# Kernel tuning notes

Hardware: AMD Instinct MI355X
Metric: run time of the kernel (lower is better)

## Reference

```python
import jax, jax.numpy as jnp
import numpy as np

K = 0.1            # manifold curvature param: points satisfy <x,x>_L = -1/K
H = 8              # num_heads
DH = 64            # head_spatial_dim
SP = 512           # spatial_dim = H*DH
SCALE = 1.0 / np.sqrt(DH)
SQRT_K = np.sqrt(K).astype(np.float32)


def _lorentz_fc(x, W, b):
    # Manifold-constrained FC: linear map to spatial coords, time recomputed
    sp = x @ W + b                                            # [..., out_spatial]
    t = jnp.sqrt(jnp.clip(1.0 / K + jnp.sum(sp * sp, axis=-1, keepdims=True), 1e-9, None))
    return jnp.concatenate([t, sp], axis=-1)


def _logmap0(p):
    # Lorentz log map at origin -> tangent spatial coords (time comp = 0)
    t, sp = p[..., :1], p[..., 1:]
    nrm = jnp.sqrt(jnp.sum(sp * sp, axis=-1, keepdims=True))
    theta = jnp.arccosh(jnp.clip(SQRT_K * t, 1.0 + 1e-7, None))
    return (theta / SQRT_K) * sp / jnp.maximum(nrm, 1e-9)


def _expmap0(u):
    nrm = jnp.sqrt(jnp.sum(u * u, axis=-1, keepdims=True))
    t = jnp.cosh(SQRT_K * nrm) / SQRT_K
    sp = jnp.sinh(SQRT_K * nrm) * u / (SQRT_K * jnp.maximum(nrm, 1e-9))
    return jnp.concatenate([t, sp], axis=-1)


def setup_inputs() -> dict:
    key = jax.random.key(0)
    ks = jax.random.split(key, 9)
    B, N = 4, 2048
    space = jax.random.normal(ks[0], (B, N, SP), dtype=jnp.float32) * 0.5
    t = jnp.sqrt(1.0 / K + jnp.sum(space * space, axis=-1, keepdims=True))
    x = jnp.concatenate([t, space], axis=-1)                  # on-manifold [B,N,513]
    s = (1 + SP) ** -0.5
    Wq = jax.random.normal(ks[1], (1 + SP, SP), dtype=jnp.float32) * s
    Wk = jax.random.normal(ks[2], (1 + SP, SP), dtype=jnp.float32) * s
    Wv = jax.random.normal(ks[3], (1 + SP, SP), dtype=jnp.float32) * s
    Wo = jax.random.normal(ks[4], (1 + SP, SP), dtype=jnp.float32) * s
    bq = jax.random.normal(ks[5], (SP,), dtype=jnp.float32) * 0.01
    bk = jax.random.normal(ks[6], (SP,), dtype=jnp.float32) * 0.01
    bv = jax.random.normal(ks[7], (SP,), dtype=jnp.float32) * 0.01
    bo = jax.random.normal(ks[8], (SP,), dtype=jnp.float32) * 0.01
    return {"x": x, "Wq": Wq, "bq": bq, "Wk": Wk, "bk": bk, "Wv": Wv, "bv": bv, "Wo": Wo, "bo": bo}


def _split_heads(p):
    # [B,N,1+H*DH] -> [B,H,N,1+DH], sharing the time component across heads
    B, N, _ = p.shape
    t = p[..., :1]                                            # [B,N,1]
    sp = p[..., 1:].reshape(B, N, H, DH)
    t = jnp.broadcast_to(t[:, :, None, :], (B, N, H, 1))
    return jnp.concatenate([t, sp], axis=-1).transpose(0, 2, 1, 3)


def reference(x, Wq, bq, Wk, bk, Wv, bv, Wo, bo):
    q = _split_heads(_lorentz_fc(x, Wq, bq))                  # [B,H,N,1+DH]
    k = _split_heads(_lorentz_fc(x, Wk, bk))
    v = _split_heads(_lorentz_fc(x, Wv, bv))
    # Lorentzian inner product scores: -q_t k_t + <q_s, k_s>
    scores = (jnp.einsum('bhnd,bhmd->bhnm', q[..., 1:], k[..., 1:])
              - jnp.einsum('bhni,bhmi->bhnm', q[..., :1], k[..., :1])) * SCALE
    attn = jax.nn.softmax(scores, axis=-1)                    # [B,H,N,N]
    # Riemannian aggregation: logmap0 -> weighted sum in tangent space -> expmap0
    v_tan = _logmap0(v)                                       # [B,H,N,DH]
    out_tan = jnp.einsum('bhnm,bhmd->bhnd', attn, v_tan)
    out = _expmap0(out_tan)                                   # [B,H,N,1+DH]
    # direct head concat: stack spatial parts, renormalize time onto manifold
    B, _, N, _ = out.shape
    space_cat = out[..., 1:].transpose(0, 2, 1, 3).reshape(B, N, H * DH)
    t_prime = jnp.sqrt(jnp.clip(1.0 / K + jnp.sum(space_cat * space_cat, axis=-1, keepdims=True), 1e-9, None))
    cat = jnp.concatenate([t_prime, space_cat], axis=-1)      # [B,N,513]
    return _lorentz_fc(cat, Wo, bo)                           # [B,N,513]
```

## Files before the change

### kernel.cpp

```cpp
#include <hip/hip_runtime.h>
#include <math.h>

#define H_    8
#define DH_   64
#define SPD   512
#define NSEQ  2048
#define BATCH 4
#define ROWS  8192
#define KDIM  513
#define INVK  10.0f
#define SQRTK 0.31622776601683794f
#define S2C   0.18033688011112043f
#define LOG2E 1.4426950408889634f
#define TKOFF 12.0f

using bf16x8 = __attribute__((ext_vector_type(8))) short;
using f32x4  = __attribute__((ext_vector_type(4))) float;
using f32x16 = __attribute__((ext_vector_type(16))) float;

static __device__ __forceinline__ short f2bf(float f){
  union { float f; unsigned u; } v; v.f = f;
  unsigned r = v.u + 0x7fffu + ((v.u >> 16) & 1u);
  return (short)(r >> 16);
}
static __device__ __forceinline__ float bf2f(short s){
  union { unsigned u; float f; } v; v.u = ((unsigned)(unsigned short)s) << 16;
  return v.f;
}
static __device__ __forceinline__ unsigned cvtpk(float lo, float hi){
  unsigned r; asm("v_cvt_pk_bf16_f32 %0, %1, %2" : "=v"(r) : "v"(lo), "v"(hi)); return r;
}
static __device__ __forceinline__ void plswapu(unsigned& a, unsigned& b){
  asm("v_permlane32_swap_b32 %0, %1" : "+v"(a), "+v"(b));
}
static __device__ __forceinline__ float exp2v(float x){
  float r; asm("v_exp_f32 %0, %1" : "=v"(r) : "v"(x)); return r;
}

#define GL16(gp, lp) __builtin_amdgcn_global_load_lds( \
    (const __attribute__((address_space(1))) void*)(gp), \
    (__attribute__((address_space(3))) void*)(lp), 16, 0, 0)

__global__ __launch_bounds__(256) void conv_kernel(const float* __restrict__ x,
                                                   const float* __restrict__ Wq,
                                                   const float* __restrict__ Wk,
                                                   const float* __restrict__ Wv,
                                                   const float* __restrict__ Wo,
                                                   short* __restrict__ xs,
                                                   short* __restrict__ WT){
  const int bid = blockIdx.x;
  if (bid < 8192){
    const int i2 = (bid * 256 + threadIdx.x) * 2;
    const int r = i2 >> 9, c = i2 & 511;
    const float a = x[(size_t)r * KDIM + 1 + c];
    const float b = x[(size_t)r * KDIM + 2 + c];
    const unsigned pk = (unsigned)(unsigned short)f2bf(a) |
                        ((unsigned)(unsigned short)f2bf(b) << 16);
    *(unsigned*)(xs + (size_t)r * SPD + c) = pk;
  } else {
    const int q = bid - 8192;
    const int wsel = q >> 10;
    const float* W = (wsel == 0) ? Wq : (wsel == 1) ? Wk : (wsel == 2) ? Wv : Wo;
    const int i = (q & 1023) * 256 + threadIdx.x;
    const int n = i >> 9, k = i & 511;
    WT[(size_t)wsel * SPD * SPD + i] = f2bf(W[(size_t)(k + 1) * SPD + n]);
  }
}

template<bool BF16OUT, int BM, bool TSQ, bool FUSESSQ>
__global__ __launch_bounds__(256) void gemm_kernel(
    const short* __restrict__ A, const short* __restrict__ WTbase,
    int sel0, int sel1, int sel2,
    const float* __restrict__ bias0, const float* __restrict__ bias1,
    const float* __restrict__ bias2,
    const float* __restrict__ W00, const float* __restrict__ W01,
    const float* __restrict__ W02,
    const float* __restrict__ tvec, long tstride,
    float* __restrict__ ssqout,
    void* __restrict__ C0, void* __restrict__ C1, void* __restrict__ C2,
    int ldc, int coff)
{
  constexpr int NREP = (BM == 128) ? 4 : 2;
  const int z = blockIdx.z;
  const int sel = (z == 0) ? sel0 : (z == 1) ? sel1 : sel2;
  const short* BT = WTbase + (size_t)sel * SPD * SPD;
  const float* bias = (z == 0) ? bias0 : (z == 1) ? bias1 : bias2;
  const float* W0 = (z == 0) ? W00 : (z == 1) ? W01 : W02;
  void* C = (z == 0) ? C0 : (z == 1) ? C1 : C2;

  __shared__ short As[BM * 32];
  __shared__ short Bs[128 * 32];

  const int tid  = threadIdx.x;
  const int lane = tid & 63;
  const int wave = tid >> 6;
  const int row0 = blockIdx.x * BM;
  const int col0 = blockIdx.y * 128;
  const int wr = (BM == 128) ? (wave >> 1) * 64 : 0;
  const int wc = (BM == 128) ? (wave & 1) * 64 : wave * 32;
  const int rA  = lane & 15;
  const int kg2 = (lane >> 4) * 16;
  const int g4  = lane >> 4;

  f32x4 acc[4][NREP] = {};

  for (int kt = 0; kt < SPD / 32; ++kt){
    __syncthreads();
    #pragma unroll
    for (int p = 0; p < BM / 64; ++p){
      const int idx = p * 256 + tid;
      const int r = idx >> 2, c4 = idx & 3;
      const int gc = (c4 ^ ((r >> 1) & 3)) * 8;
      GL16(A + (size_t)(row0 + r) * SPD + kt * 32 + gc, (char*)As + idx * 16);
    }
    #pragma unroll
    for (int p = 0; p < 2; ++p){
      const int idx = p * 256 + tid;
      const int r = idx >> 2, c4 = idx & 3;
      const int gc = (c4 ^ ((r >> 1) & 3)) * 8;
      GL16(BT + (size_t)(col0 + r) * SPD + kt * 32 + gc, (char*)Bs + idx * 16);
    }
    asm volatile("s_waitcnt vmcnt(0)" ::: "memory");
    __syncthreads();
    bf16x8 af[4], bfr[NREP];
    #pragma unroll
    for (int m = 0; m < 4; ++m){
      const int r = wr + m * 16 + rA;
      af[m] = *(const bf16x8*)((const char*)As + ((r * 64 + kg2) ^ (((r >> 1) & 3) << 4)));
    }
    #pragma unroll
    for (int n = 0; n < NREP; ++n){
      const int r = wc + n * 16 + rA;
      bfr[n] = *(const bf16x8*)((const char*)Bs + ((r * 64 + kg2) ^ (((r >> 1) & 3) << 4)));
    }
    #pragma unroll
    for (int m = 0; m < 4; ++m)
      #pragma unroll
      for (int n = 0; n < NREP; ++n)
        acc[m][n] = __builtin_amdgcn_mfma_f32_16x16x32_bf16(af[m], bfr[n], acc[m][n], 0, 0, 0);
  }

  float trow[4][4];
  #pragma unroll
  for (int m = 0; m < 4; ++m)
    #pragma unroll
    for (int j = 0; j < 4; ++j){
      const float raw = tvec[(size_t)(row0 + wr + m * 16 + g4 * 4 + j) * tstride];
      trow[m][j] = TSQ ? sqrtf(fmaxf(INVK + raw, 1e-9f)) : raw;
    }

  float rssq[4][4];
  #pragma unroll
  for (int m = 0; m < 4; ++m)
    #pragma unroll
    for (int j = 0; j < 4; ++j) rssq[m][j] = 0.f;

  #pragma unroll
  for (int m = 0; m < 4; ++m){
    const int row = row0 + wr + m * 16 + g4 * 4;
    #pragma unroll
    for (int n = 0; n < NREP; ++n){
      const int col = col0 + wc + n * 16 + rA;
      const float bv = bias[col];
      const float w0 = W0[col];
      #pragma unroll
      for (int j = 0; j < 4; ++j){
        const float v = acc[m][n][j] + trow[m][j] * w0 + bv;
        if (FUSESSQ) rssq[m][j] += v * v;
        if (BF16OUT) ((short*)C)[(size_t)(row + j) * SPD + col] = f2bf(v);
        else         ((float*)C)[(size_t)(row + j) * ldc + coff + col] = v;
      }
    }
  }
  if (FUSESSQ){
    #pragma unroll
    for (int m = 0; m < 4; ++m)
      #pragma unroll
      for (int j = 0; j < 4; ++j){
        float s = rssq[m][j];
        s += __shfl_xor(s, 1, 64);
        s += __shfl_xor(s, 2, 64);
        s += __shfl_xor(s, 4, 64);
        s += __shfl_xor(s, 8, 64);
        if (rA == 0) atomicAdd(&ssqout[row0 + wr + m * 16 + g4 * 4 + j], s);
      }
  }
}

__global__ __launch_bounds__(256) void postqkv_kernel(
    const short* __restrict__ qb, const short* __restrict__ kb,
    const short* __restrict__ vb, float* __restrict__ tq,
    unsigned* __restrict__ tkpk, short* __restrict__ vtT)
{
  const int tid = threadIdx.x;
  const int lane = tid & 63;
  const int wv = tid >> 6;
  const int row0 = blockIdx.x * 8 + wv * 2;
  const int b = blockIdx.x >> 8;

  #pragma unroll
  for (int i = 0; i < 2; ++i){
    const int row = row0 + i;
    const int n = row & (NSEQ - 1);
    {
      union { bf16x8 v; short e[8]; } u;
      u.v = *(const bf16x8*)(qb + (size_t)row * SPD + lane * 8);
      float s = 0.f;
      #pragma unroll
      for (int j = 0; j < 8; ++j){ const float f = bf2f(u.e[j]); s += f * f; }
      #pragma unroll
      for (int m = 1; m <= 32; m <<= 1) s += __shfl_xor(s, m, 64);
      if (lane == 0) tq[row] = sqrtf(INVK + s);
    }
    {
      union { bf16x8 v; short e[8]; } u;
      u.v = *(const bf16x8*)(kb + (size_t)row * SPD + lane * 8);
      float s = 0.f;
      #pragma unroll
      for (int j = 0; j < 8; ++j){ const float f = bf2f(u.e[j]); s += f * f; }
      #pragma unroll
      for (int m = 1; m <= 32; m <<= 1) s += __shfl_xor(s, m, 64);
      if (lane == 0){
        const float tkm = sqrtf(INVK + s) - TKOFF;
        const short bhi = f2bf(tkm);
        const short blo = f2bf(tkm - bf2f(bhi));
        tkpk[row] = (unsigned)(unsigned short)bhi | ((unsigned)(unsigned short)blo << 16);
      }
    }
    {
      union { bf16x8 v; short e[8]; } u;
      u.v = *(const bf16x8*)(vb + (size_t)row * SPD + lane * 8);
      float f[8]; float sh = 0.f;
      #pragma unroll
      for (int j = 0; j < 8; ++j){ f[j] = bf2f(u.e[j]); sh += f[j] * f[j]; }
      sh += __shfl_xor(sh, 1, 64);
      sh += __shfl_xor(sh, 2, 64);
      sh += __shfl_xor(sh, 4, 64);
      float tot = sh;
      tot += __shfl_xor(tot, 8, 64);
      tot += __shfl_xor(tot, 16, 64);
      tot += __shfl_xor(tot, 32, 64);
      const float tv = sqrtf(INVK + tot);
      const float av = fmaxf(SQRTK * tv, 1.0f + 1e-7f);
      const float theta = __logf(av + sqrtf(av * av - 1.0f));
      const float fac = theta * (1.0f / SQRTK);
      const float inv = fac / fmaxf(sqrtf(sh), 1e-9f);
      const int h = lane >> 3;
      const int d0 = (lane & 7) * 8;
      short* dst = vtT + ((size_t)((b * H_ + h) * DH_ + d0)) * NSEQ + n;
      #pragma unroll
      for (int j = 0; j < 8; ++j) dst[(size_t)j * NSEQ] = f2bf(inv * f[j]);
    }
  }
}

__global__ __launch_bounds__(256) void attn_kernel(
    const short* __restrict__ qb, const short* __restrict__ kb,
    const short* __restrict__ vtT, const float* __restrict__ tqg,
    const unsigned* __restrict__ tkpk, short* __restrict__ catb,
    float* __restrict__ tps)
{
  int bid = blockIdx.x;
  bid = (bid & 7) * 64 + (bid >> 3);
  const int qt = bid & 15;
  const int bh = bid >> 4;
  const int b = bh >> 3, h = bh & 7;
  const int q0 = qt * 128;
  const int tid = threadIdx.x;
  const int lane = tid & 63;
  const int w = tid >> 6;
  const int l31 = lane & 31;
  const int hi = lane >> 5;
  const int rsw = (l31 & 7) << 4;

  __shared__ short Ks[2][64 * 64];
  __shared__ short Vs[2][64 * 64];
  __shared__ float lred[4][32];
  __shared__ unsigned tks[NSEQ];

  const int qrow = q0 + w * 32 + l31;
  bf16x8 qf[4];
  {
    const short* qptr = qb + (size_t)(b * NSEQ + qrow) * SPD + h * DH_ + hi * 8;
    #pragma unroll
    for (int s = 0; s < 4; ++s){
      union { bf16x8 v; short e[8]; } u;
      u.v = *(const bf16x8*)(qptr + s * 16);
      #pragma unroll
      for (int j = 0; j < 8; ++j) u.e[j] = f2bf(bf2f(u.e[j]) * S2C);
      qf[s] = u.v;
    }
  }
  bf16x8 qf4;
  {
    const float a = -S2C * tqg[b * NSEQ + qrow];
    const short ahi = f2bf(a);
    const short alo = f2bf(a - bf2f(ahi));
    union { unsigned u[4]; bf16x8 v; } q4;
    q4.u[0] = hi ? 0u : ((unsigned)(unsigned short)ahi | ((unsigned)(unsigned short)alo << 16));
    q4.u[1] = hi ? 0u : (unsigned)(unsigned short)ahi;
    q4.u[2] = 0; q4.u[3] = 0;
    qf4 = q4.v;
  }
  bf16x8 onesB;
  {
    const unsigned val = (l31 == 0) ? 0x3f803f80u : 0u;
    union { unsigned u[4]; bf16x8 v; } ob;
    ob.u[0] = val; ob.u[1] = val; ob.u[2] = val; ob.u[3] = val;
    onesB = ob.v;
  }

  {
    const unsigned* tsrc = tkpk + b * NSEQ + tid * 8;
    *(uint4*)&tks[tid * 8]     = *(const uint4*)tsrc;
    *(uint4*)&tks[tid * 8 + 4] = *(const uint4*)(tsrc + 4);
  }

  int koff[2][4];
  #pragma unroll
  for (int f = 0; f < 2; ++f)
    #pragma unroll
    for (int s = 0; s < 4; ++s)
      koff[f][s] = (f * 32 + l31) * 128 + ((s * 32 + hi * 16) ^ rsw);

  const int rB = tid >> 3;
  const int c0 = (tid & 7) * 16;
  const int cc = c0 ^ ((rB & 7) << 4);
  const short* kbase = kb + (size_t)(b * NSEQ) * SPD + h * DH_;
  const short* vbase = vtT + (size_t)(bh * DH_) * NSEQ;

  uint4 kA0, kA1, vA0, vA1;
  uint4 kB0, kB1, vB0, vB1;

#define LOADA(m0) do{ \
    kA0 = *(const uint4*)(kbase + (size_t)((m0) + rB) * SPD + (c0 >> 1)); \
    kA1 = *(const uint4*)(kbase + (size_t)((m0) + 32 + rB) * SPD + (c0 >> 1)); \
    vA0 = *(const uint4*)(vbase + (size_t)rB * NSEQ + (m0) + (c0 >> 1)); \
    vA1 = *(const uint4*)(vbase + (size_t)(32 + rB) * NSEQ + (m0) + (c0 >> 1)); }while(0)
#define LOADB(m0) do{ \
    kB0 = *(const uint4*)(kbase + (size_t)((m0) + rB) * SPD + (c0 >> 1)); \
    kB1 = *(const uint4*)(kbase + (size_t)((m0) + 32 + rB) * SPD + (c0 >> 1)); \
    vB0 = *(const uint4*)(vbase + (size_t)rB * NSEQ + (m0) + (c0 >> 1)); \
    vB1 = *(const uint4*)(vbase + (size_t)(32 + rB) * NSEQ + (m0) + (c0 >> 1)); }while(0)
#define WRITEA(buf) do{ \
    *(uint4*)((char*)Ks[buf] + rB * 128 + cc) = kA0; \
    *(uint4*)((char*)Ks[buf] + (32 + rB) * 128 + cc) = kA1; \
    *(uint4*)((char*)Vs[buf] + rB * 128 + cc) = vA0; \
    *(uint4*)((char*)Vs[buf] + (32 + rB) * 128 + cc) = vA1; }while(0)
#define WRITEB(buf) do{ \
    *(uint4*)((char*)Ks[buf] + rB * 128 + cc) = kB0; \
    *(uint4*)((char*)Ks[buf] + (32 + rB) * 128 + cc) = kB1; \
    *(uint4*)((char*)Vs[buf] + rB * 128 + cc) = vB0; \
    *(uint4*)((char*)Vs[buf] + (32 + rB) * 128 + cc) = vB1; }while(0)
#define BARRIER() asm volatile("s_waitcnt lgkmcnt(0)\n\ts_barrier" ::: "memory")
#define WAITV4()  asm volatile("s_waitcnt vmcnt(4)" ::: "memory")
#define WAITV0()  asm volatile("s_waitcnt vmcnt(0)" ::: "memory")

  f32x16 o[2] = {};
  f32x16 lacc = {};
  const f32x16 z16 = {};

  auto KAUG = [&](unsigned pk)->bf16x8{
    union { unsigned u[4]; bf16x8 v; } ka;
    ka.u[0] = hi ? 0u : ((pk & 0xFFFFu) | (pk << 16));
    ka.u[1] = hi ? 0u : (pk >> 16);
    ka.u[2] = 0; ka.u[3] = 0;
    return ka.v;
  };

  auto COMPUTE = [&](const char* Kc, const char* Vc, int m0){
    const unsigned pk0 = tks[m0 + l31];
    const unsigned pk1 = tks[m0 + 32 + l31];

    f32x16 sacc[2];
    __builtin_amdgcn_s_setprio(1);
    #pragma unroll
    for (int f = 0; f < 2; ++f){
      {
        const bf16x8 kf = *(const bf16x8*)(Kc + koff[f][0]);
        sacc[f] = __builtin_amdgcn_mfma_f32_32x32x16_bf16(kf, qf[0], z16, 0, 0, 0);
      }
      #pragma unroll
      for (int s = 1; s < 4; ++s){
        const bf16x8 kf = *(const bf16x8*)(Kc + koff[f][s]);
        sacc[f] = __builtin_amdgcn_mfma_f32_32x32x16_bf16(kf, qf[s], sacc[f], 0, 0, 0);
      }
    }
    sacc[0] = __builtin_amdgcn_mfma_f32_32x32x16_bf16(KAUG(pk0), qf4, sacc[0], 0, 0, 0);
    sacc[1] = __builtin_amdgcn_mfma_f32_32x32x16_bf16(KAUG(pk1), qf4, sacc[1], 0, 0, 0);
    __builtin_amdgcn_s_setprio(0);

    #pragma unroll
    for (int f = 0; f < 2; ++f)
      #pragma unroll
      for (int e = 0; e < 16; ++e)
        sacc[f][e] = exp2v(sacc[f][e]);

    bf16x8 pa[4];
    #pragma unroll
    for (int f = 0; f < 2; ++f)
      #pragma unroll
      for (int g16 = 0; g16 < 2; ++g16){
        const int bse = g16 * 8;
        unsigned A0 = cvtpk(sacc[f][bse + 0], sacc[f][bse + 1]);
        unsigned A1 = cvtpk(sacc[f][bse + 2], sacc[f][bse + 3]);
        unsigned B0 = cvtpk(sacc[f][bse + 4], sacc[f][bse + 5]);
        unsigned B1 = cvtpk(sacc[f][bse + 6], sacc[f][bse + 7]);
        plswapu(A0, B0);
        plswapu(A1, B1);
        union { unsigned u[4]; bf16x8 v; } pu;
        pu.u[0] = A0; pu.u[1] = A1; pu.u[2] = B0; pu.u[3] = B1;
        pa[f * 2 + g16] = pu.v;
      }

    __builtin_amdgcn_s_setprio(1);
    #pragma unroll
    for (int db = 0; db < 2; ++db)
      #pragma unroll
      for (int ks = 0; ks < 4; ++ks){
        const bf16x8 vf = *(const bf16x8*)(Vc + koff[db][ks]);
        o[db] = __builtin_amdgcn_mfma_f32_32x32x16_bf16(pa[ks], vf, o[db], 0, 0, 0);
      }
    #pragma unroll
    for (int ks = 0; ks < 4; ++ks)
      lacc = __builtin_amdgcn_mfma_f32_32x32x16_bf16(pa[ks], onesB, lacc, 0, 0, 0);
    __builtin_amdgcn_s_setprio(0);
  };

  LOADA(0);
  WAITV0();
  WRITEA(0);
  __syncthreads();
  LOADB(64);

  const int NT = NSEQ / 64;
  #pragma unroll 1
  for (int t = 0; t < NT; t += 2){
    const int m0 = t * 64;
    if (t + 2 < NT) LOADA(m0 + 128);
    COMPUTE((const char*)Ks[0], (const char*)Vs[0], m0);
    if (t + 2 < NT) WAITV4(); else WAITV0();
    WRITEB(1);
    BARRIER();
    if (t + 3 < NT) LOADB(m0 + 192);
    COMPUTE((const char*)Ks[1], (const char*)Vs[1], m0 + 64);
    if (t + 2 < NT){
      if (t + 3 < NT) WAITV4(); else WAITV0();
      WRITEA(0);
    }
    BARRIER();
  }

  if (l31 == 0){
    #pragma unroll
    for (int e = 0; e < 16; ++e)
      lred[w][(e & 3) + 8 * (e >> 2) + 4 * hi] = lacc[e];
  }
  asm volatile("s_waitcnt lgkmcnt(0)" ::: "memory");
  f32x4 lv[4];
  #pragma unroll
  for (int g = 0; g < 4; ++g) lv[g] = *(const f32x4*)&lred[w][8 * g + 4 * hi];

  const int brow = b * NSEQ + q0 + w * 32;
  const size_t obase = (size_t)brow * SPD + h * DH_ + l31;
  #pragma unroll
  for (int e = 0; e < 16; ++e){
    const float linv = __builtin_amdgcn_rcpf(lv[e >> 2][e & 3]);
    const float ov0 = o[0][e] * linv;
    const float ov1 = o[1][e] * linv;
    float ss = ov0 * ov0 + ov1 * ov1;
    #pragma unroll
    for (int off = 16; off; off >>= 1) ss += __shfl_xor(ss, off, 64);
    const float nrm = sqrtf(ss);
    const float e2 = exp2f(SQRTK * nrm * LOG2E);
    const float einv = __builtin_amdgcn_rcpf(e2);
    const float fac = (e2 - einv) * 0.5f * __builtin_amdgcn_rcpf(SQRTK * fmaxf(nrm, 1e-9f));
    const int crow = (e & 3) + 8 * (e >> 2) + 4 * hi;
    catb[obase + (size_t)crow * SPD]      = f2bf(fac * ov0);
    catb[obase + (size_t)crow * SPD + 32] = f2bf(fac * ov1);
    if (l31 == 0) atomicAdd(&tps[brow + crow], fac * fac * ss);
  }
#undef LOADA
#undef LOADB
#undef WRITEA
#undef WRITEB
#undef BARRIER
#undef WAITV4
#undef WAITV0
}

__global__ __launch_bounds__(256) void fin2_kernel(float* __restrict__ out,
                                                   const float* __restrict__ tos){
  const int r = blockIdx.x * 256 + threadIdx.x;
  out[(size_t)r * KDIM] = sqrtf(fmaxf(INVK + tos[r], 1e-9f));
}

extern "C" void kernel_launch(void* const* d_in, const int* in_sizes, int n_in,
                              void* d_out, int out_size, void* d_ws, size_t ws_size,
                              hipStream_t stream)
{
  (void)in_sizes; (void)n_in; (void)out_size; (void)ws_size;
  const float* x  = (const float*)d_in[0];
  const float* Wq = (const float*)d_in[1];
  const float* bq = (const float*)d_in[2];
  const float* Wk = (const float*)d_in[3];
  const float* bk = (const float*)d_in[4];
  const float* Wv = (const float*)d_in[5];
  const float* bv = (const float*)d_in[6];
  const float* Wo = (const float*)d_in[7];
  const float* bo = (const float*)d_in[8];
  float* out = (float*)d_out;

  char* p = (char*)d_ws;
  short* xs   = (short*)p; p += (size_t)ROWS * SPD * 2;
  short* WT   = (short*)p; p += (size_t)4 * SPD * SPD * 2;
  short* qb   = (short*)p; p += (size_t)ROWS * SPD * 2;
  short* kb   = (short*)p; p += (size_t)ROWS * SPD * 2;
  short* vb   = (short*)p; p += (size_t)ROWS * SPD * 2;
  short* vtT  = (short*)p; p += (size_t)ROWS * SPD * 2;
  float* tq   = (float*)p; p += (size_t)ROWS * 4;
  unsigned* tkpk = (unsigned*)p; p += (size_t)ROWS * 4;
  short* catb = (short*)p; p += (size_t)ROWS * SPD * 2;
  float* tps  = (float*)p; p += (size_t)ROWS * 4;
  float* tos  = (float*)p; p += (size_t)ROWS * 4;

  hipMemsetAsync(tps, 0, (size_t)2 * ROWS * 4, stream);
  conv_kernel<<<8192 + 4096, 256, 0, stream>>>(x, Wq, Wk, Wv, Wo, xs, WT);
  gemm_kernel<true, 128, false, false><<<dim3(64, 4, 3), 256, 0, stream>>>(
      xs, WT, 0, 1, 2, bq, bk, bv, Wq, Wk, Wv, x, (long)KDIM, nullptr,
      qb, kb, vb, SPD, 0);
  postqkv_kernel<<<1024, 256, 0, stream>>>(qb, kb, vb, tq, tkpk, vtT);
  attn_kernel<<<512, 256, 0, stream>>>(qb, kb, vtT, tq, tkpk, catb, tps);
  gemm_kernel<false, 64, true, true><<<dim3(128, 4, 1), 256, 0, stream>>>(
      catb, WT, 3, 3, 3, bo, bo, bo, Wo, Wo, Wo, tps, 1L, tos,
      out, out, out, KDIM, 1);
  fin2_kernel<<<ROWS / 256, 256, 0, stream>>>(out, tos);
}
```

Before: 149.0 us.

## Double-buffer GEMM tiles, tile weight transpose via LDS, move time norm out of attention

The GEMM kernel now uses double-buffered LDS tiles. The next k-tile is issued before the current one is consumed, with one barrier per step, so load latency can overlap the MFMAs. The weight conversion now transposes 64x64 tiles through shared memory, giving coalesced reads and writes and fewer blocks. The attention kernel no longer does per-row atomicAdds for the head-concat squared norm; a new tp_kernel recomputes it from the bf16 output and applies the sqrt, and minor K/V offset precomputation is removed. Risks: an extra kernel launch, a norm computed from bf16-rounded values, and the removed s_waitcnt before the barrier, which may leave GL16 loads unsynchronized.

Result: faster. 145.3 us (-2.5%).

```diff
diff --git a/kernel.cpp b/kernel.cpp
--- a/kernel.cpp
+++ b/kernel.cpp
@@ -49,8 +49,9 @@
                                                    short* __restrict__ xs,
                                                    short* __restrict__ WT){
   const int bid = blockIdx.x;
+  const int tid = threadIdx.x;
   if (bid < 8192){
-    const int i2 = (bid * 256 + threadIdx.x) * 2;
+    const int i2 = (bid * 256 + tid) * 2;
     const int r = i2 >> 9, c = i2 & 511;
     const float a = x[(size_t)r * KDIM + 1 + c];
     const float b = x[(size_t)r * KDIM + 2 + c];
@@ -58,16 +59,31 @@
                         ((unsigned)(unsigned short)f2bf(b) << 16);
     *(unsigned*)(xs + (size_t)r * SPD + c) = pk;
   } else {
+    __shared__ float lds[64][65];
     const int q = bid - 8192;
-    const int wsel = q >> 10;
+    const int wsel = q >> 6;
     const float* W = (wsel == 0) ? Wq : (wsel == 1) ? Wk : (wsel == 2) ? Wv : Wo;
-    const int i = (q & 1023) * 256 + threadIdx.x;
-    const int n = i >> 9, k = i & 511;
-    WT[(size_t)wsel * SPD * SPD + i] = f2bf(W[(size_t)(k + 1) * SPD + n]);
-  }
-}
-
-template<bool BF16OUT, int BM, bool TSQ, bool FUSESSQ>
+    const int rem = q & 63;
+    const int kt0 = (rem >> 3) << 6;
+    const int nt0 = (rem & 7) << 6;
+    const int wv = tid >> 6;
+    const int ln = tid & 63;
+    #pragma unroll
+    for (int e = 0; e < 16; ++e){
+      const int kk = e * 4 + wv;
+      lds[kk][ln] = W[(size_t)(kt0 + kk + 1) * SPD + nt0 + ln];
+    }
+    __syncthreads();
+    short* dst = WT + (size_t)wsel * SPD * SPD;
+    #pragma unroll
+    for (int e = 0; e < 16; ++e){
+      const int nn = e * 4 + wv;
+      dst[(size_t)(nt0 + nn) * SPD + kt0 + ln] = f2bf(lds[ln][nn]);
+    }
+  }
+}
+
+template<bool BF16OUT, int BM, bool FUSESSQ>
 __global__ __launch_bounds__(256) void gemm_kernel(
     const short* __restrict__ A, const short* __restrict__ WTbase,
     int sel0, int sel1, int sel2,
@@ -88,8 +104,8 @@
   const float* W0 = (z == 0) ? W00 : (z == 1) ? W01 : W02;
   void* C = (z == 0) ? C0 : (z == 1) ? C1 : C2;
 
-  __shared__ short As[BM * 32];
-  __shared__ short Bs[128 * 32];
+  __shared__ short As[2][BM * 32];
+  __shared__ short Bs[2][128 * 32];
 
   const int tid  = threadIdx.x;
   const int lane = tid & 63;
@@ -102,52 +118,56 @@
   const int kg2 = (lane >> 4) * 16;
   const int g4  = lane >> 4;
 
-  f32x4 acc[4][NREP] = {};
-
-  for (int kt = 0; kt < SPD / 32; ++kt){
-    __syncthreads();
+  auto STAGE = [&](int buf, int kt){
     #pragma unroll
     for (int p = 0; p < BM / 64; ++p){
       const int idx = p * 256 + tid;
       const int r = idx >> 2, c4 = idx & 3;
       const int gc = (c4 ^ ((r >> 1) & 3)) * 8;
-      GL16(A + (size_t)(row0 + r) * SPD + kt * 32 + gc, (char*)As + idx * 16);
+      GL16(A + (size_t)(row0 + r) * SPD + kt * 32 + gc, (char*)As[buf] + idx * 16);
     }
     #pragma unroll
     for (int p = 0; p < 2; ++p){
       const int idx = p * 256 + tid;
       const int r = idx >> 2, c4 = idx & 3;
       const int gc = (c4 ^ ((r >> 1) & 3)) * 8;
-      GL16(BT + (size_t)(col0 + r) * SPD + kt * 32 + gc, (char*)Bs + idx * 16);
-    }
-    asm volatile("s_waitcnt vmcnt(0)" ::: "memory");
-    __syncthreads();
+      GL16(BT + (size_t)(col0 + r) * SPD + kt * 32 + gc, (char*)Bs[buf] + idx * 16);
+    }
+  };
+
+  f32x4 acc[4][NREP] = {};
+
+  STAGE(0, 0);
+  __syncthreads();
+
+  for (int kt = 0; kt < SPD / 32; ++kt){
+    const int cur = kt & 1;
+    if (kt + 1 < SPD / 32) STAGE(cur ^ 1, kt + 1);
     bf16x8 af[4], bfr[NREP];
     #pragma unroll
     for (int m = 0; m < 4; ++m){
       const int r = wr + m * 16 + rA;
-      af[m] = *(const bf16x8*)((const char*)As + ((r * 64 + kg2) ^ (((r >> 1) & 3) << 4)));
+      af[m] = *(const bf16x8*)((const char*)As[cur] + ((r * 64 + kg2) ^ (((r >> 1) & 3) << 4)));
     }
     #pragma unroll
     for (int n = 0; n < NREP; ++n){
       const int r = wc + n * 16 + rA;
-      bfr[n] = *(const bf16x8*)((const char*)Bs + ((r * 64 + kg2) ^ (((r >> 1) & 3) << 4)));
+      bfr[n] = *(const bf16x8*)((const char*)Bs[cur] + ((r * 64 + kg2) ^ (((r >> 1) & 3) << 4)));
     }
     #pragma unroll
     for (int m = 0; m < 4; ++m)
       #pragma unroll
       for (int n = 0; n < NREP; ++n)
         acc[m][n] = __builtin_amdgcn_mfma_f32_16x16x32_bf16(af[m], bfr[n], acc[m][n], 0, 0, 0);
+    __syncthreads();
   }
 
   float trow[4][4];
   #pragma unroll
   for (int m = 0; m < 4; ++m)
     #pragma unroll
-    for (int j = 0; j < 4; ++j){
-      const float raw = tvec[(size_t)(row0 + wr + m * 16 + g4 * 4 + j) * tstride];
-      trow[m][j] = TSQ ? sqrtf(fmaxf(INVK + raw, 1e-9f)) : raw;
-    }
+    for (int j = 0; j < 4; ++j)
+      trow[m][j] = tvec[(size_t)(row0 + wr + m * 16 + g4 * 4 + j) * tstride];
 
   float rssq[4][4];
   #pragma unroll
@@ -257,8 +277,7 @@
 __global__ __launch_bounds__(256) void attn_kernel(
     const short* __restrict__ qb, const short* __restrict__ kb,
     const short* __restrict__ vtT, const float* __restrict__ tqg,
-    const unsigned* __restrict__ tkpk, short* __restrict__ catb,
-    float* __restrict__ tps)
+    const unsigned* __restrict__ tkpk, short* __restrict__ catb)
 {
   int bid = blockIdx.x;
   bid = (bid & 7) * 64 + (bid >> 3);
@@ -315,13 +334,6 @@
     *(uint4*)&tks[tid * 8]     = *(const uint4*)tsrc;
     *(uint4*)&tks[tid * 8 + 4] = *(const uint4*)(tsrc + 4);
   }
-
-  int koff[2][4];
-  #pragma unroll
-  for (int f = 0; f < 2; ++f)
-    #pragma unroll
-    for (int s = 0; s < 4; ++s)
-      koff[f][s] = (f * 32 + l31) * 128 + ((s * 32 + hi * 16) ^ rsw);
 
   const int rB = tid >> 3;
   const int c0 = (tid & 7) * 16;
@@ -358,7 +370,6 @@
 
   f32x16 o[2] = {};
   f32x16 lacc = {};
-  const f32x16 z16 = {};
 
   auto KAUG = [&](unsigned pk)->bf16x8{
     union { unsigned u[4]; bf16x8 v; } ka;
@@ -372,17 +383,14 @@
     const unsigned pk0 = tks[m0 + l31];
     const unsigned pk1 = tks[m0 + 32 + l31];
 
-    f32x16 sacc[2];
+    f32x16 sacc[2] = {};
     __builtin_amdgcn_s_setprio(1);
     #pragma unroll
     for (int f = 0; f < 2; ++f){
-      {
-        const bf16x8 kf = *(const bf16x8*)(Kc + koff[f][0]);
-        sacc[f] = __builtin_amdgcn_mfma_f32_32x32x16_bf16(kf, qf[0], z16, 0, 0, 0);
-      }
-      #pragma unroll
-      for (int s = 1; s < 4; ++s){
-        const bf16x8 kf = *(const bf16x8*)(Kc + koff[f][s]);
+      const int rowb = (f * 32 + l31) * 128;
+      #pragma unroll
+      for (int s = 0; s < 4; ++s){
+        const bf16x8 kf = *(const bf16x8*)(Kc + rowb + ((s * 32 + hi * 16) ^ rsw));
         sacc[f] = __builtin_amdgcn_mfma_f32_32x32x16_bf16(kf, qf[s], sacc[f], 0, 0, 0);
       }
     }
@@ -415,12 +423,14 @@
 
     __builtin_amdgcn_s_setprio(1);
     #pragma unroll
-    for (int db = 0; db < 2; ++db)
+    for (int db = 0; db < 2; ++db){
+      const int rowb = (db * 32 + l31) * 128;
       #pragma unroll
       for (int ks = 0; ks < 4; ++ks){
-        const bf16x8 vf = *(const bf16x8*)(Vc + koff[db][ks]);
+        const bf16x8 vf = *(const bf16x8*)(Vc + rowb + ((ks * 32 + hi * 16) ^ rsw));
         o[db] = __builtin_amdgcn_mfma_f32_32x32x16_bf16(pa[ks], vf, o[db], 0, 0, 0);
       }
+    }
     #pragma unroll
     for (int ks = 0; ks < 4; ++ks)
       lacc = __builtin_amdgcn_mfma_f32_32x32x16_bf16(pa[ks], onesB, lacc, 0, 0, 0);
@@ -461,8 +471,7 @@
   #pragma unroll
   for (int g = 0; g < 4; ++g) lv[g] = *(const f32x4*)&lred[w][8 * g + 4 * hi];
 
-  const int brow = b * NSEQ + q0 + w * 32;
-  const size_t obase = (size_t)brow * SPD + h * DH_ + l31;
+  const size_t obase = (size_t)(b * NSEQ + q0 + w * 32) * SPD + h * DH_ + l31;
   #pragma unroll
   for (int e = 0; e < 16; ++e){
     const float linv = __builtin_amdgcn_rcpf(lv[e >> 2][e & 3]);
@@ -478,7 +487,6 @@
     const int crow = (e & 3) + 8 * (e >> 2) + 4 * hi;
     catb[obase + (size_t)crow * SPD]      = f2bf(fac * ov0);
     catb[obase + (size_t)crow * SPD + 32] = f2bf(fac * ov1);
-    if (l31 == 0) atomicAdd(&tps[brow + crow], fac * fac * ss);
   }
 #undef LOADA
 #undef LOADB
@@ -487,6 +495,20 @@
 #undef BARRIER
 #undef WAITV4
 #undef WAITV0
+}
+
+__global__ __launch_bounds__(256) void tp_kernel(const short* __restrict__ catb,
+                                                 float* __restrict__ tps){
+  const int lane = threadIdx.x & 63;
+  const int row = blockIdx.x * 4 + (threadIdx.x >> 6);
+  union { bf16x8 v; short e[8]; } u;
+  u.v = *(const bf16x8*)(catb + (size_t)row * SPD + lane * 8);
+  float s = 0.f;
+  #pragma unroll
+  for (int j = 0; j < 8; ++j){ const float f = bf2f(u.e[j]); s += f * f; }
+  #pragma unroll
+  for (int m = 1; m <= 32; m <<= 1) s += __shfl_xor(s, m, 64);
+  if (lane == 0) tps[row] = sqrtf(fmaxf(INVK + s, 1e-9f));
 }
 
 __global__ __launch_bounds__(256) void fin2_kernel(float* __restrict__ out,
@@ -524,14 +546,15 @@
   float* tps  = (float*)p; p += (size_t)ROWS * 4;
   float* tos  = (float*)p; p += (size_t)ROWS * 4;
 
-  hipMemsetAsync(tps, 0, (size_t)2 * ROWS * 4, stream);
-  conv_kernel<<<8192 + 4096, 256, 0, stream>>>(x, Wq, Wk, Wv, Wo, xs, WT);
-  gemm_kernel<true, 128, false, false><<<dim3(64, 4, 3), 256, 0, stream>>>(
+  hipMemsetAsync(tos, 0, (size_t)ROWS * 4, stream);
+  conv_kernel<<<8192 + 256, 256, 0, stream>>>(x, Wq, Wk, Wv, Wo, xs, WT);
+  gemm_kernel<true, 128, false><<<dim3(64, 4, 3), 256, 0, stream>>>(
       xs, WT, 0, 1, 2, bq, bk, bv, Wq, Wk, Wv, x, (long)KDIM, nullptr,
       qb, kb, vb, SPD, 0);
   postqkv_kernel<<<1024, 256, 0, stream>>>(qb, kb, vb, tq, tkpk, vtT);
-  attn_kernel<<<512, 256, 0, stream>>>(qb, kb, vtT, tq, tkpk, catb, tps);
-  gemm_kernel<false, 64, true, true><<<dim3(128, 4, 1), 256, 0, stream>>>(
+  attn_kernel<<<512, 256, 0, stream>>>(qb, kb, vtT, tq, tkpk, catb);
+  tp_kernel<<<ROWS / 4, 256, 0, stream>>>(catb, tps);
+  gemm_kernel<false, 64, true><<<dim3(128, 4, 1), 256, 0, stream>>>(
       catb, WT, 3, 3, 3, bo, bo, bo, Wo, Wo, Wo, tps, 1L, tos,
       out, out, out, KDIM, 1);
   fin2_kernel<<<ROWS / 256, 256, 0, stream>>>(out, tos);
```
